# Kernel tuning notes

Hardware: AMD Instinct MI355X
Metric: run time of the kernel (lower is better)

The kernel has to match this reference:

```python
import jax, jax.numpy as jnp
import numpy as np

L_COORD = 5.0
L_NOOBJ = 0.5


def _iou(box, tbox):
    """IoU of center-format boxes (cx, cy, w, h); broadcasts over leading dims."""
    ax1 = box[..., 0] - box[..., 2] / 2
    ay1 = box[..., 1] - box[..., 3] / 2
    ax2 = box[..., 0] + box[..., 2] / 2
    ay2 = box[..., 1] + box[..., 3] / 2
    bx1 = tbox[..., 0] - tbox[..., 2] / 2
    by1 = tbox[..., 1] - tbox[..., 3] / 2
    bx2 = tbox[..., 0] + tbox[..., 2] / 2
    by2 = tbox[..., 1] + tbox[..., 3] / 2
    iw = jnp.maximum(jnp.minimum(ax2, bx2) - jnp.maximum(ax1, bx1), 0.0)
    ih = jnp.maximum(jnp.minimum(ay2, by2) - jnp.maximum(ay1, by1), 0.0)
    inter = iw * ih
    union = box[..., 2] * box[..., 3] + tbox[..., 2] * tbox[..., 3] - inter
    return inter / jnp.maximum(union, 1e-10)


def setup_inputs() -> dict:
    key = jax.random.key(0)
    k1, k2, k3 = jax.random.split(key, 3)
    B, S, C = 16384, 7, 30
    pred = jax.random.uniform(k1, (B, S, S, C), dtype=jnp.float32)
    target = jax.random.uniform(k2, (B, S, S, C), dtype=jnp.float32)
    obj = (jax.random.uniform(k3, (B, S, S)) > 0.8).astype(jnp.float32)
    target = target.at[..., 4].set(obj)
    target = target.at[..., 9].set(obj)
    return {"pred": pred, "target": target}


def reference(pred, target):
    B = pred.shape[0]
    objf = (target[..., 4] == 1.0).astype(pred.dtype)   # [B,7,7]
    noobjf = 1.0 - objf

    # two predicted boxes per cell: [B,7,7,2,5]
    pboxes = pred[..., :10].reshape(pred.shape[:3] + (2, 5))
    tbox = target[..., :4]                               # [B,7,7,4] (box1 of target, as in the loop)

    # IoU of both predicted boxes vs the target box; detached as in the original
    iou = jax.lax.stop_gradient(_iou(pboxes[..., :4], tbox[..., None, :]))  # [B,7,7,2]
    # original tie-break: iou1 > iou2 -> box 0, else box 1
    best = jnp.where(iou[..., 0] > iou[..., 1], 0, 1)    # [B,7,7]
    sel = jax.nn.one_hot(best, 2, dtype=pred.dtype)      # responder mask [B,7,7,2]
    wbox = jnp.einsum('bijk,bijkc->bijc', sel, pboxes)   # responder box [B,7,7,5]
    wiou = jnp.max(iou, axis=-1)                         # winner IoU = new conf target

    # localization loss (sum over object cells)
    xy = jnp.sum((wbox[..., :2] - tbox[..., :2]) ** 2, axis=-1)
    wh = jnp.sum((jnp.sqrt(wbox[..., 2:4]) - jnp.sqrt(tbox[..., 2:4])) ** 2, axis=-1)
    loc_loss = jnp.sum((xy + wh) * objf)

    # responder confidence loss vs (detached) IoU
    conf_loss_obj = jnp.sum(((wbox[..., 4] - wiou) ** 2) * objf)

    # class cross-entropy, mean over object cells (nn.CrossEntropyLoss default)
    logp = jax.nn.log_softmax(pred[..., 10:30], axis=-1)
    cls_t = jnp.argmax(target[..., 10:30], axis=-1)
    ce = -jnp.take_along_axis(logp, cls_t[..., None], axis=-1)[..., 0]
    n_obj = jnp.maximum(jnp.sum(objf), 1.0)
    cls_loss = jnp.sum(ce * objf) / n_obj

    # no-object confidence loss on both box slots (channels 4 and 9)
    conf_loss_no_obj = jnp.sum(((pred[..., 4] - target[..., 4]) ** 2 +
                                (pred[..., 9] - target[..., 9]) ** 2) * noobjf)

    total = (L_COORD * loc_loss + conf_loss_obj +
             L_NOOBJ * conf_loss_no_obj + cls_loss) / B
    return total, loc_loss, conf_loss_obj, conf_loss_no_obj, cls_loss
```

## Files before the change

### kernel.cpp

```cpp
#include <hip/hip_runtime.h>
#include <stdint.h>

#define L_COORD 5.0f
#define L_NOOBJ 0.5f

#define BLOCK 256
#define CPB   256
#define CHUNK_FLOATS (CPB * 30)
#define KB_PER_TENSOR 30

__device__ __forceinline__ float iou_one(float cx, float cy, float w, float h,
                                         float tx, float ty, float tw, float th) {
    float ax1 = cx - w * 0.5f, ay1 = cy - h * 0.5f;
    float ax2 = cx + w * 0.5f, ay2 = cy + h * 0.5f;
    float bx1 = tx - tw * 0.5f, by1 = ty - th * 0.5f;
    float bx2 = tx + tw * 0.5f, by2 = ty + th * 0.5f;
    float iw = fmaxf(fminf(ax2, bx2) - fmaxf(ax1, bx1), 0.0f);
    float ih = fmaxf(fminf(ay2, by2) - fmaxf(ay1, by1), 0.0f);
    float inter = iw * ih;
    float uni = w * h + tw * th - inter;
    return inter / fmaxf(uni, 1e-10f);
}

__global__ __launch_bounds__(BLOCK) void yolo_loss_partial(
    const float* __restrict__ pred, const float* __restrict__ target,
    float* __restrict__ partial,
    int nchunks)
{
    __shared__ float smp[CHUNK_FLOATS];
    __shared__ float smt[CHUNK_FLOATS];

    const int wid  = threadIdx.x >> 6;
    const int lane = threadIdx.x & 63;

    float loc = 0.0f, cobj = 0.0f, cnoobj = 0.0f, clsn = 0.0f, nobj = 0.0f;

    for (int chunk = blockIdx.x; chunk < nchunks; chunk += gridDim.x) {
        const size_t fbase = (size_t)chunk * CHUNK_FLOATS;

        for (int c = wid; c < KB_PER_TENSOR; c += 4) {
            const float* gp = pred   + fbase + c * 256 + lane * 4;
            const float* gt = target + fbase + c * 256 + lane * 4;
            __builtin_amdgcn_global_load_lds(
                (const __attribute__((address_space(1))) void*)gp,
                (__attribute__((address_space(3))) void*)&smp[c * 256], 16, 0, 0);
            __builtin_amdgcn_global_load_lds(
                (const __attribute__((address_space(1))) void*)gt,
                (__attribute__((address_space(3))) void*)&smt[c * 256], 16, 0, 0);
        }
        asm volatile("s_waitcnt vmcnt(0)" ::: "memory");
        __syncthreads();

        {
            const float2* p2 = reinterpret_cast<const float2*>(&smp[threadIdx.x * 30]);
            const float2* t2 = reinterpret_cast<const float2*>(&smt[threadIdx.x * 30]);

            float p[30], t[30];
#pragma unroll
            for (int k = 0; k < 15; ++k) {
                float2 v = p2[k];
                p[2 * k] = v.x; p[2 * k + 1] = v.y;
            }
#pragma unroll
            for (int k = 0; k < 15; ++k) {
                float2 v = t2[k];
                t[2 * k] = v.x; t[2 * k + 1] = v.y;
            }

            float objf = (t[4] == 1.0f) ? 1.0f : 0.0f;
            float noobjf = 1.0f - objf;

            float iou0 = iou_one(p[0], p[1], p[2], p[3], t[0], t[1], t[2], t[3]);
            float iou1 = iou_one(p[5], p[6], p[7], p[8], t[0], t[1], t[2], t[3]);

            bool b0 = iou0 > iou1;
            float wx  = b0 ? p[0] : p[5];
            float wy  = b0 ? p[1] : p[6];
            float ww  = b0 ? p[2] : p[7];
            float whh = b0 ? p[3] : p[8];
            float wc  = b0 ? p[4] : p[9];
            float wiou = fmaxf(iou0, iou1);

            float dx = wx - t[0], dy = wy - t[1];
            float xy = dx * dx + dy * dy;
            float dw = sqrtf(ww) - sqrtf(t[2]);
            float dh = sqrtf(whh) - sqrtf(t[3]);
            float wh = dw * dw + dh * dh;
            loc += (xy + wh) * objf;

            float dc = wc - wiou;
            cobj += dc * dc * objf;

            float m = p[10];
#pragma unroll
            for (int k = 11; k < 30; ++k) m = fmaxf(m, p[k]);
            float s = 0.0f;
#pragma unroll
            for (int k = 10; k < 30; ++k) s += __expf(p[k] - m);

            float tm = t[10];
            float psel = p[10];
#pragma unroll
            for (int k = 11; k < 30; ++k) {
                bool gt = t[k] > tm;
                tm = gt ? t[k] : tm;
                psel = gt ? p[k] : psel;
            }
            float ce = (m + __logf(s)) - psel;
            clsn += ce * objf;
            nobj += objf;

            float d4 = p[4] - t[4], d9 = p[9] - t[9];
            cnoobj += (d4 * d4 + d9 * d9) * noobjf;
        }

        __syncthreads();
    }

#pragma unroll
    for (int off = 32; off > 0; off >>= 1) {
        loc    += __shfl_down(loc, off);
        cobj   += __shfl_down(cobj, off);
        cnoobj += __shfl_down(cnoobj, off);
        clsn   += __shfl_down(clsn, off);
        nobj   += __shfl_down(nobj, off);
    }

    __shared__ float sm[4][5];
    if (lane == 0) {
        sm[wid][0] = loc; sm[wid][1] = cobj; sm[wid][2] = cnoobj;
        sm[wid][3] = clsn; sm[wid][4] = nobj;
    }
    __syncthreads();
    if (threadIdx.x == 0) {
        float a0 = 0.f, a1 = 0.f, a2 = 0.f, a3 = 0.f, a4 = 0.f;
#pragma unroll
        for (int w = 0; w < 4; ++w) {
            a0 += sm[w][0]; a1 += sm[w][1]; a2 += sm[w][2];
            a3 += sm[w][3]; a4 += sm[w][4];
        }
        int g = gridDim.x, b = blockIdx.x;
        partial[0 * g + b] = a0;
        partial[1 * g + b] = a1;
        partial[2 * g + b] = a2;
        partial[3 * g + b] = a3;
        partial[4 * g + b] = a4;
    }
}

__global__ __launch_bounds__(256) void yolo_reduce(
    const float* __restrict__ partial, int n, float* __restrict__ out, float invB)
{
    float v0 = 0.f, v1 = 0.f, v2 = 0.f, v3 = 0.f, v4 = 0.f;
    for (int i = threadIdx.x; i < n; i += 256) {
        v0 += partial[0 * n + i];
        v1 += partial[1 * n + i];
        v2 += partial[2 * n + i];
        v3 += partial[3 * n + i];
        v4 += partial[4 * n + i];
    }
#pragma unroll
    for (int off = 32; off > 0; off >>= 1) {
        v0 += __shfl_down(v0, off);
        v1 += __shfl_down(v1, off);
        v2 += __shfl_down(v2, off);
        v3 += __shfl_down(v3, off);
        v4 += __shfl_down(v4, off);
    }
    __shared__ float sm[4][5];
    int lane = threadIdx.x & 63;
    int wid = threadIdx.x >> 6;
    if (lane == 0) {
        sm[wid][0] = v0; sm[wid][1] = v1; sm[wid][2] = v2;
        sm[wid][3] = v3; sm[wid][4] = v4;
    }
    __syncthreads();
    if (threadIdx.x == 0) {
        float loc = 0.f, cobj = 0.f, cnoobj = 0.f, clsum = 0.f, nobj = 0.f;
#pragma unroll
        for (int w = 0; w < 4; ++w) {
            loc += sm[w][0]; cobj += sm[w][1]; cnoobj += sm[w][2];
            clsum += sm[w][3]; nobj += sm[w][4];
        }
        float nn = fmaxf(nobj, 1.0f);
        float cls = clsum / nn;
        float total = (L_COORD * loc + cobj + L_NOOBJ * cnoobj + cls) * invB;
        out[0] = total;
        out[1] = loc;
        out[2] = cobj;
        out[3] = cnoobj;
        out[4] = cls;
    }
}

extern "C" void kernel_launch(void* const* d_in, const int* in_sizes, int n_in,
                              void* d_out, int out_size, void* d_ws, size_t ws_size,
                              hipStream_t stream) {
    const float* pred = (const float*)d_in[0];
    const float* target = (const float*)d_in[1];
    float* out = (float*)d_out;
    float* partial = (float*)d_ws;

    int ncells = in_sizes[0] / 30;
    int B = ncells / 49;
    int nchunks = ncells / CPB;

    int blocks = nchunks;
    int maxb = (int)(ws_size / (5 * sizeof(float)));
    if (blocks > maxb) blocks = maxb;
    if (blocks < 1) blocks = 1;

    yolo_loss_partial<<<blocks, BLOCK, 0, stream>>>(pred, target, partial, nchunks);
    yolo_reduce<<<1, 256, 0, stream>>>(partial, blocks, out, 1.0f / (float)B);
}
```

Measured before the change: 40.21 us.

## Double-buffer LDS loads in a persistent grid and handle tail cells in reduce

Switches to a persistent grid of at most 256 blocks that loops over chunks. LDS is double-buffered so the global-to-LDS loads for the next chunk are issued while the current chunk is computed, replacing the load-wait-compute-sync pattern. Each wave now loads half of one tensor, and a partial vmcnt wait plus raw barriers replace __syncthreads. Leftover cells that do not fill a whole chunk are now processed in the reduce kernel. The risks are that 256 blocks with about 120KB of LDS each may underfill the GPU's CUs, and that the barrier and wait logic is subtle.

```diff
diff --git a/kernel.cpp b/kernel.cpp
--- a/kernel.cpp
+++ b/kernel.cpp
@@ -7,19 +7,72 @@
 #define BLOCK 256
 #define CPB   256
 #define CHUNK_FLOATS (CPB * 30)
-#define KB_PER_TENSOR 30
-
-__device__ __forceinline__ float iou_one(float cx, float cy, float w, float h,
-                                         float tx, float ty, float tw, float th) {
-    float ax1 = cx - w * 0.5f, ay1 = cy - h * 0.5f;
-    float ax2 = cx + w * 0.5f, ay2 = cy + h * 0.5f;
-    float bx1 = tx - tw * 0.5f, by1 = ty - th * 0.5f;
-    float bx2 = tx + tw * 0.5f, by2 = ty + th * 0.5f;
-    float iw = fmaxf(fminf(ax2, bx2) - fmaxf(ax1, bx1), 0.0f);
-    float ih = fmaxf(fminf(ay2, by2) - fmaxf(ay1, by1), 0.0f);
-    float inter = iw * ih;
-    float uni = w * h + tw * th - inter;
-    return inter / fmaxf(uni, 1e-10f);
+
+__device__ __forceinline__ void cell_terms(const float* __restrict__ p,
+                                           const float* __restrict__ t,
+                                           float& loc, float& cobj, float& cnoobj,
+                                           float& clsn, float& nobj)
+{
+    float objf = (t[4] == 1.0f) ? 1.0f : 0.0f;
+    float noobjf = 1.0f - objf;
+
+    float tx1 = t[0] - t[2] * 0.5f, ty1 = t[1] - t[3] * 0.5f;
+    float tx2 = t[0] + t[2] * 0.5f, ty2 = t[1] + t[3] * 0.5f;
+    float tarea = t[2] * t[3];
+
+    float a0x1 = p[0] - p[2] * 0.5f, a0y1 = p[1] - p[3] * 0.5f;
+    float a0x2 = p[0] + p[2] * 0.5f, a0y2 = p[1] + p[3] * 0.5f;
+    float iw0 = fmaxf(fminf(a0x2, tx2) - fmaxf(a0x1, tx1), 0.0f);
+    float ih0 = fmaxf(fminf(a0y2, ty2) - fmaxf(a0y1, ty1), 0.0f);
+    float in0 = iw0 * ih0;
+    float iou0 = in0 / fmaxf(p[2] * p[3] + tarea - in0, 1e-10f);
+
+    float a1x1 = p[5] - p[7] * 0.5f, a1y1 = p[6] - p[8] * 0.5f;
+    float a1x2 = p[5] + p[7] * 0.5f, a1y2 = p[6] + p[8] * 0.5f;
+    float iw1 = fmaxf(fminf(a1x2, tx2) - fmaxf(a1x1, tx1), 0.0f);
+    float ih1 = fmaxf(fminf(a1y2, ty2) - fmaxf(a1y1, ty1), 0.0f);
+    float in1 = iw1 * ih1;
+    float iou1 = in1 / fmaxf(p[7] * p[8] + tarea - in1, 1e-10f);
+
+    bool b0 = iou0 > iou1;
+    float wx  = b0 ? p[0] : p[5];
+    float wy  = b0 ? p[1] : p[6];
+    float ww  = b0 ? p[2] : p[7];
+    float whh = b0 ? p[3] : p[8];
+    float wc  = b0 ? p[4] : p[9];
+    float wiou = fmaxf(iou0, iou1);
+
+    float dx = wx - t[0], dy = wy - t[1];
+    float xy = dx * dx + dy * dy;
+    float dw = sqrtf(ww) - sqrtf(t[2]);
+    float dh = sqrtf(whh) - sqrtf(t[3]);
+    float wh = dw * dw + dh * dh;
+    loc += (xy + wh) * objf;
+
+    float dc = wc - wiou;
+    cobj += dc * dc * objf;
+
+    float m = p[10];
+#pragma unroll
+    for (int k = 11; k < 30; ++k) m = fmaxf(m, p[k]);
+    float s = 0.0f;
+#pragma unroll
+    for (int k = 10; k < 30; ++k) s += __expf(p[k] - m);
+
+    float tm = t[10];
+    float psel = p[10];
+#pragma unroll
+    for (int k = 11; k < 30; ++k) {
+        bool gt = t[k] > tm;
+        tm = gt ? t[k] : tm;
+        psel = gt ? p[k] : psel;
+    }
+    float ce = (m + __logf(s)) - psel;
+    clsn += ce * objf;
+    nobj += objf;
+
+    float d4 = p[4] - t[4], d9 = p[9] - t[9];
+    cnoobj += (d4 * d4 + d9 * d9) * noobjf;
 }
 
 __global__ __launch_bounds__(BLOCK) void yolo_loss_partial(
@@ -27,34 +80,51 @@
     float* __restrict__ partial,
     int nchunks)
 {
-    __shared__ float smp[CHUNK_FLOATS];
-    __shared__ float smt[CHUNK_FLOATS];
+    __shared__ float lds[2][2][CHUNK_FLOATS];
 
     const int wid  = threadIdx.x >> 6;
     const int lane = threadIdx.x & 63;
+    const int G    = gridDim.x;
+
+    const float* sbase  = (wid & 2) ? target : pred;
+    const int tsel      = wid >> 1;
+    const int sub0      = (wid & 1) * 15;
 
     float loc = 0.0f, cobj = 0.0f, cnoobj = 0.0f, clsn = 0.0f, nobj = 0.0f;
 
-    for (int chunk = blockIdx.x; chunk < nchunks; chunk += gridDim.x) {
-        const size_t fbase = (size_t)chunk * CHUNK_FLOATS;
-
-        for (int c = wid; c < KB_PER_TENSOR; c += 4) {
-            const float* gp = pred   + fbase + c * 256 + lane * 4;
-            const float* gt = target + fbase + c * 256 + lane * 4;
+    int chunk = blockIdx.x;
+    int cur = 0;
+
+    if (chunk < nchunks) {
+        const float* src = sbase + (size_t)chunk * CHUNK_FLOATS + sub0 * 256 + lane * 4;
+        float* dst = &lds[0][tsel][sub0 * 256];
+#pragma unroll
+        for (int i = 0; i < 15; ++i)
             __builtin_amdgcn_global_load_lds(
-                (const __attribute__((address_space(1))) void*)gp,
-                (__attribute__((address_space(3))) void*)&smp[c * 256], 16, 0, 0);
-            __builtin_amdgcn_global_load_lds(
-                (const __attribute__((address_space(1))) void*)gt,
-                (__attribute__((address_space(3))) void*)&smt[c * 256], 16, 0, 0);
-        }
-        asm volatile("s_waitcnt vmcnt(0)" ::: "memory");
-        __syncthreads();
+                (const __attribute__((address_space(1))) void*)(src + i * 256),
+                (__attribute__((address_space(3))) void*)(dst + i * 256), 16, 0, 0);
+    }
+
+    for (; chunk < nchunks; chunk += G) {
+        int next = chunk + G;
+        if (next < nchunks) {
+            const float* src = sbase + (size_t)next * CHUNK_FLOATS + sub0 * 256 + lane * 4;
+            float* dst = &lds[cur ^ 1][tsel][sub0 * 256];
+#pragma unroll
+            for (int i = 0; i < 15; ++i)
+                __builtin_amdgcn_global_load_lds(
+                    (const __attribute__((address_space(1))) void*)(src + i * 256),
+                    (__attribute__((address_space(3))) void*)(dst + i * 256), 16, 0, 0);
+            asm volatile("s_waitcnt vmcnt(15)" ::: "memory");
+        } else {
+            asm volatile("s_waitcnt vmcnt(0)" ::: "memory");
+        }
+        __builtin_amdgcn_s_barrier();
+        __builtin_amdgcn_sched_barrier(0);
 
         {
-            const float2* p2 = reinterpret_cast<const float2*>(&smp[threadIdx.x * 30]);
-            const float2* t2 = reinterpret_cast<const float2*>(&smt[threadIdx.x * 30]);
-
+            const float2* p2 = reinterpret_cast<const float2*>(&lds[cur][0][threadIdx.x * 30]);
+            const float2* t2 = reinterpret_cast<const float2*>(&lds[cur][1][threadIdx.x * 30]);
             float p[30], t[30];
 #pragma unroll
             for (int k = 0; k < 15; ++k) {
@@ -66,55 +136,12 @@
                 float2 v = t2[k];
                 t[2 * k] = v.x; t[2 * k + 1] = v.y;
             }
-
-            float objf = (t[4] == 1.0f) ? 1.0f : 0.0f;
-            float noobjf = 1.0f - objf;
-
-            float iou0 = iou_one(p[0], p[1], p[2], p[3], t[0], t[1], t[2], t[3]);
-            float iou1 = iou_one(p[5], p[6], p[7], p[8], t[0], t[1], t[2], t[3]);
-
-            bool b0 = iou0 > iou1;
-            float wx  = b0 ? p[0] : p[5];
-            float wy  = b0 ? p[1] : p[6];
-            float ww  = b0 ? p[2] : p[7];
-            float whh = b0 ? p[3] : p[8];
-            float wc  = b0 ? p[4] : p[9];
-            float wiou = fmaxf(iou0, iou1);
-
-            float dx = wx - t[0], dy = wy - t[1];
-            float xy = dx * dx + dy * dy;
-            float dw = sqrtf(ww) - sqrtf(t[2]);
-            float dh = sqrtf(whh) - sqrtf(t[3]);
-            float wh = dw * dw + dh * dh;
-            loc += (xy + wh) * objf;
-
-            float dc = wc - wiou;
-            cobj += dc * dc * objf;
-
-            float m = p[10];
-#pragma unroll
-            for (int k = 11; k < 30; ++k) m = fmaxf(m, p[k]);
-            float s = 0.0f;
-#pragma unroll
-            for (int k = 10; k < 30; ++k) s += __expf(p[k] - m);
-
-            float tm = t[10];
-            float psel = p[10];
-#pragma unroll
-            for (int k = 11; k < 30; ++k) {
-                bool gt = t[k] > tm;
-                tm = gt ? t[k] : tm;
-                psel = gt ? p[k] : psel;
-            }
-            float ce = (m + __logf(s)) - psel;
-            clsn += ce * objf;
-            nobj += objf;
-
-            float d4 = p[4] - t[4], d9 = p[9] - t[9];
-            cnoobj += (d4 * d4 + d9 * d9) * noobjf;
-        }
-
-        __syncthreads();
+            cell_terms(p, t, loc, cobj, cnoobj, clsn, nobj);
+        }
+
+        __builtin_amdgcn_sched_barrier(0);
+        __builtin_amdgcn_s_barrier();
+        cur ^= 1;
     }
 
 #pragma unroll
@@ -149,7 +176,10 @@
 }
 
 __global__ __launch_bounds__(256) void yolo_reduce(
-    const float* __restrict__ partial, int n, float* __restrict__ out, float invB)
+    const float* __restrict__ partial, int n,
+    const float* __restrict__ pred, const float* __restrict__ target,
+    int tail0, int ncells,
+    float* __restrict__ out, float invB)
 {
     float v0 = 0.f, v1 = 0.f, v2 = 0.f, v3 = 0.f, v4 = 0.f;
     for (int i = threadIdx.x; i < n; i += 256) {
@@ -159,6 +189,12 @@
         v3 += partial[3 * n + i];
         v4 += partial[4 * n + i];
     }
+    for (int c = tail0 + threadIdx.x; c < ncells; c += 256) {
+        float p[30], t[30];
+#pragma unroll
+        for (int k = 0; k < 30; ++k) { p[k] = pred[(size_t)c * 30 + k]; t[k] = target[(size_t)c * 30 + k]; }
+        cell_terms(p, t, v0, v1, v2, v3, v4);
+    }
 #pragma unroll
     for (int off = 32; off > 0; off >>= 1) {
         v0 += __shfl_down(v0, off);
@@ -204,12 +240,14 @@
     int ncells = in_sizes[0] / 30;
     int B = ncells / 49;
     int nchunks = ncells / CPB;
-
-    int blocks = nchunks;
+    int tail0 = nchunks * CPB;
+
+    int blocks = nchunks < 256 ? nchunks : 256;
     int maxb = (int)(ws_size / (5 * sizeof(float)));
     if (blocks > maxb) blocks = maxb;
     if (blocks < 1) blocks = 1;
 
     yolo_loss_partial<<<blocks, BLOCK, 0, stream>>>(pred, target, partial, nchunks);
-    yolo_reduce<<<1, 256, 0, stream>>>(partial, blocks, out, 1.0f / (float)B);
-}
+    yolo_reduce<<<1, 256, 0, stream>>>(partial, blocks, pred, target, tail0, ncells,
+                                       out, 1.0f / (float)B);
+}
```

Measured after the change: 41.42 us. +3.0%, slower.
